# Kernel tuning notes

Measured on AMD Instinct MI355X. Metric: run time of the kernel, lower is better.

Reference implementation:

```python
import jax, jax.numpy as jnp
import numpy as np

EPS = 1e-5

def setup_inputs() -> dict:
    key = jax.random.key(0)
    ks = jax.random.split(key, 12)
    b, C, Hx = 8, 1024, 28          # x: (b, C, Hx, Hx); y: (b, C//2, 2*Hx, 2*Hx)
    C2 = C // 2
    r = C2 // 7                      # fc bottleneck = 73
    f32 = jnp.float32
    inp = {
        'y': jax.random.normal(ks[0], (b, C2, 2*Hx, 2*Hx), f32),
        'x': jax.random.normal(ks[1], (b, C, Hx, Hx), f32),
        'fc1_w': jax.random.normal(ks[2], (r, C2), f32) * 0.02,
        'fc2_w': jax.random.normal(ks[3], (C2, r), f32) * 0.02,
        'conv_w': jax.random.normal(ks[4], (C2, C, 1, 1), f32) * 0.02,
        'conv_b': jnp.zeros((C2,), f32),
        'conv1_w': jax.random.normal(ks[5], (C2, C2 * 4, 1, 1), f32) * 0.02,
        'conv1_b': jnp.zeros((C2,), f32),
        'bn_gamma': jnp.ones((C2,), f32),
        'bn_beta': jnp.zeros((C2,), f32),
        'bn_mean': jnp.zeros((C2,), f32),
        'bn_var': jnp.ones((C2,), f32),
        'dw_w': jax.random.normal(ks[6], (C, 1, 3, 3), f32) * 0.1,  # depthwise, groups=C
        'dw_b': jnp.zeros((C,), f32),
    }
    return inp

def reference(y, x, fc1_w, fc2_w, conv_w, conv_b, conv1_w, conv1_b,
              bn_gamma, bn_beta, bn_mean, bn_var, dw_w, dw_b):
    def bn(t):  # BatchNorm2d in eval mode (running stats); same bn module reused twice
        return (t - bn_mean[:, None, None]) * jax.lax.rsqrt(bn_var[:, None, None] + EPS) \
               * bn_gamma[:, None, None] + bn_beta[:, None, None]
    # SE channel attention on y
    s = jnp.mean(y, axis=(2, 3))                              # (b, C2) GAP
    s = jax.nn.relu(s @ fc1_w.T) @ fc2_w.T                    # bias-free FCs
    y1 = y * jax.nn.sigmoid(s)[:, :, None, None]
    # depthwise 3x3 conv on x
    x1 = jax.lax.conv_general_dilated(
        x, dw_w, (1, 1), ((1, 1), (1, 1)),
        feature_group_count=x.shape[1],
        dimension_numbers=('NCHW', 'OIHW', 'NCHW')) + dw_b[None, :, None, None]
    # np.cov per (b, c) map: rows are variables, ddof=1 -> (Xc @ Xc^T)/(W-1)
    Wn = x1.shape[-1]
    xc = x1 - jnp.mean(x1, axis=-1, keepdims=True)
    x2 = jnp.einsum('bchw,bcgw->bchg', xc, xc) / (Wn - 1)     # (b, C, H, H)
    # 1x1 conv C->C2, bn, sigmoid
    x2 = jnp.einsum('bchw,oc->bohw', x2, conv_w[:, :, 0, 0]) + conv_b[None, :, None, None]
    x2 = jax.nn.sigmoid(bn(x2))
    # bilinear upsample x2 (half-pixel == torch align_corners=False)
    def up2(t):
        bb, cc, hh, ww = t.shape
        return jax.image.resize(t, (bb, cc, 2 * hh, 2 * ww), method='bilinear')
    x_up = up2(x)
    x2_up = up2(x2)
    cat = jnp.concatenate([y1, x2_up, x_up], axis=1)          # (b, 4*C2, 2H, 2W)
    out = jnp.einsum('bchw,oc->bohw', cat, conv1_w[:, :, 0, 0]) + conv1_b[None, :, None, None]
    return jax.nn.relu(bn(out))
```

## Files before the change

kernel.cpp:

```cpp
#include <hip/hip_runtime.h>
#include <math.h>

#define EPSV 1e-5f
#define B 8
#define C 1024
#define C2 512
#define RK 73
#define HW 784
#define QW 3136

typedef __attribute__((ext_vector_type(8))) short bf16x8;
typedef __attribute__((ext_vector_type(4))) float f32x4;

__device__ __forceinline__ unsigned short f2bf(float f) {
    unsigned u = __float_as_uint(f);
    return (unsigned short)((u + 0x7fffu + ((u >> 16) & 1u)) >> 16);
}
__device__ __forceinline__ float ld_f(const float* p) { return *p; }
__device__ __forceinline__ float ld_f(const unsigned short* p) {
    return __uint_as_float(((unsigned)*p) << 16);
}

__global__ void zero_s0(float* __restrict__ s0) {
    s0[blockIdx.x * 256 + threadIdx.x] = 0.f;
}

__global__ void se_fc_kernel(const float* __restrict__ s0,
                             const float* __restrict__ fc1_w,
                             const float* __restrict__ fc2_w,
                             float* __restrict__ att) {
    int b = blockIdx.x;
    __shared__ float sv[C2];
    __shared__ float hv[RK];
    for (int i = threadIdx.x; i < C2; i += 256) sv[i] = s0[b * C2 + i] * (1.0f / QW);
    __syncthreads();
    if (threadIdx.x < RK) {
        float acc = 0.f;
        const float4* wr4 = (const float4*)(fc1_w + threadIdx.x * C2);
        const float4* sv4 = (const float4*)sv;
#pragma unroll 16
        for (int k = 0; k < C2 / 4; ++k) {
            float4 w4 = wr4[k], s4 = sv4[k];
            acc += w4.x * s4.x + w4.y * s4.y + w4.z * s4.z + w4.w * s4.w;
        }
        hv[threadIdx.x] = fmaxf(acc, 0.f);
    }
    __syncthreads();
    for (int o = threadIdx.x; o < C2; o += 256) {
        float acc = 0.f;
        const float* wr = fc2_w + o * RK;
#pragma unroll
        for (int j = 0; j < RK; ++j) acc += wr[j] * hv[j];
        att[b * C2 + o] = 1.f / (1.f + expf(-acc));
    }
}

__global__ void dwcov_kernel(const float* __restrict__ x,
                             const float* __restrict__ dw_w,
                             const float* __restrict__ dw_b,
                             unsigned short* __restrict__ cov) {
    int bc = blockIdx.x;
    int c = bc & (C - 1);
    __shared__ float xs[HW];
    __shared__ float x1[HW];
    __shared__ float rm[28];
    const float* px = x + (size_t)bc * HW;
    for (int i = threadIdx.x; i < HW; i += 256) xs[i] = px[i];
    float wk[9];
#pragma unroll
    for (int j = 0; j < 9; ++j) wk[j] = dw_w[c * 9 + j];
    float bias = dw_b[c];
    __syncthreads();
    for (int p = threadIdx.x; p < HW; p += 256) {
        int h = p / 28, w = p - h * 28;
        float acc = bias;
#pragma unroll
        for (int dh = 0; dh < 3; ++dh) {
            int hh = h + dh - 1;
            if (hh < 0 || hh >= 28) continue;
#pragma unroll
            for (int dw = 0; dw < 3; ++dw) {
                int ww = w + dw - 1;
                if (ww < 0 || ww >= 28) continue;
                acc += xs[hh * 28 + ww] * wk[dh * 3 + dw];
            }
        }
        x1[p] = acc;
    }
    __syncthreads();
    if (threadIdx.x < 28) {
        float s = 0.f;
        for (int w = 0; w < 28; ++w) s += x1[threadIdx.x * 28 + w];
        rm[threadIdx.x] = s * (1.f / 28.f);
    }
    __syncthreads();
    unsigned short* pc = cov + (size_t)bc * HW;
    for (int p = threadIdx.x; p < HW; p += 256) {
        int h = p / 28, g = p - h * 28;
        float mh = rm[h], mg = rm[g];
        float acc = 0.f;
        for (int w = 0; w < 28; ++w)
            acc += (x1[h * 28 + w] - mh) * (x1[g * 28 + w] - mg);
        pc[p] = f2bf(acc * (1.f / 27.f));
    }
}

__global__ void pack_w(const float* __restrict__ conv_w, const float* __restrict__ conv_b,
                       const float* __restrict__ conv1_w, const float* __restrict__ conv1_b,
                       const float* __restrict__ bn_g, const float* __restrict__ bn_b,
                       const float* __restrict__ bn_m, const float* __restrict__ bn_v,
                       const float* __restrict__ att,
                       unsigned short* __restrict__ w0b, unsigned short* __restrict__ w1y,
                       unsigned short* __restrict__ w1pT,
                       float* __restrict__ sA, float* __restrict__ sB0, float* __restrict__ sB1) {
    int o = blockIdx.x, t = threadIdx.x;
    for (int i = t; i < C; i += 256) w0b[(size_t)o * C + i] = f2bf(conv_w[(size_t)o * C + i]);
    for (int i = t; i < 1536; i += 256) w1pT[(size_t)o * 1536 + i] = f2bf(conv1_w[(size_t)o * 2048 + 512 + i]);
#pragma unroll
    for (int b = 0; b < B; ++b)
        for (int c2 = t; c2 < C2; c2 += 256)
            w1y[((size_t)b * C2 + o) * C2 + c2] = f2bf(conv1_w[(size_t)o * 2048 + c2] * att[b * C2 + c2]);
    if (t == 0) {
        float sc = rsqrtf(bn_v[o] + EPSV) * bn_g[o];
        float bi = bn_b[o] - bn_m[o] * sc;
        sA[o] = sc;
        sB0[o] = conv_b[o] * sc + bi;
        sB1[o] = conv1_b[o] * sc + bi;
    }
}

template<typename ST, bool GAP>
__global__ __launch_bounds__(256)
void transpose_pass(const ST* __restrict__ src, unsigned short* __restrict__ dst,
                    float* __restrict__ s0,
                    int rows, int cols, int dpitch, int doff) {
    int b = blockIdx.z;
    int c0 = blockIdx.y * 64, p0 = blockIdx.x * 64;
    __shared__ float ts[64][65];
    int tid = threadIdx.x;
    int pl = tid & 63, r0 = tid >> 6;
    const ST* sb = src + ((size_t)b * rows + c0) * cols + p0;
    if (p0 + pl < cols) {
#pragma unroll
        for (int j = 0; j < 16; ++j) {
            int cl = r0 + j * 4;
            ts[cl][pl] = ld_f(&sb[(size_t)cl * cols + pl]);
        }
    }
    __syncthreads();
    int pl2b = tid >> 3, cl0 = (tid & 7) * 8;
#pragma unroll
    for (int j = 0; j < 2; ++j) {
        int pl2 = pl2b + j * 32;
        if (p0 + pl2 < cols) {
            unsigned short pk[8];
#pragma unroll
            for (int i = 0; i < 8; ++i) pk[i] = f2bf(ts[cl0 + i][pl2]);
            *(uint4*)&dst[((size_t)b * cols + p0 + pl2) * dpitch + doff + c0 + cl0] = *(uint4*)pk;
        }
    }
    if (GAP) {
        if (tid < 64) {
            float s = 0.f;
#pragma unroll
            for (int i = 0; i < 64; ++i) s += ts[tid][i];
            atomicAdd(&s0[b * rows + c0 + tid], s);
        }
    }
}

template<int MODE, int K>
__global__ __launch_bounds__(256)
void mfma_gemm(const unsigned short* __restrict__ wpk,
               const unsigned short* __restrict__ bsrc,
               const unsigned short* __restrict__ Pb,
               const float* __restrict__ sA, const float* __restrict__ sB,
               void* __restrict__ outv) {
    constexpr int NIT = K / 32;
    constexpr int NT  = (MODE == 2) ? 49 : 98;
    constexpr int QN = NT >> 3, REM = NT & 7;
    int bx = blockIdx.x;
    int r = bx & 7, ii = bx >> 3;
    int og = ii & 7, s = ii >> 3;
    int cnt = QN + (r < REM ? 1 : 0);
    if (s >= cnt) return;
    int t = (r < REM ? r * (QN + 1) : REM * (QN + 1) + (r - REM) * QN) + s;
    int o0 = og * 64;
    int n0 = t * 64;
    int b = blockIdx.z;
    union SM {
        struct { __align__(16) unsigned short Wt[2][2048]; __align__(16) unsigned short At[2][2048]; } s;
        float pt[(MODE == 2) ? 64 * 84 : 4];
    };
    __shared__ SM sm;
    int tid = threadIdx.x;
    int lane = tid & 63, wv = tid >> 6;
    int ln = lane & 15, quad = lane >> 4;
    int o_w = (wv >> 1) * 32, q_w = (wv & 1) * 32;
    int swr = tid >> 2, swk = (tid & 3) * 8;
    int stw = swr * 32 + (((tid & 3) ^ ((swr >> 1) & 3)) << 3);
    int rq  = (quad ^ ((ln >> 1) & 3)) << 3;
    const unsigned short* wp = (MODE == 2) ? wpk + (size_t)b * C2 * C2 : wpk;
    const unsigned short* wg = wp + (size_t)(o0 + swr) * K + swk;
    const unsigned short* bg = bsrc + ((size_t)((MODE == 2) ? b * QW : 0) + n0 + swr) * K + swk;

    uint4 stA_a, stA_b, stB_a, stB_b;

#define LD_STAGE(P, CH) {                                                   \
        P##_a = *(const uint4*)(wg + (size_t)(CH) * 32);                    \
        P##_b = *(const uint4*)(bg + (size_t)(CH) * 32); }

#define ST_STAGE(P, BUF) {                                                  \
        *(uint4*)&sm.s.Wt[BUF][stw] = P##_a;                                \
        *(uint4*)&sm.s.At[BUF][stw] = P##_b; }

#define GEMM_BODY(BUF, P, CHW, CHL) {                                               \
        bf16x8 af0 = *(const bf16x8*)&sm.s.Wt[BUF][(o_w + ln) * 32 + rq];           \
        bf16x8 af1 = *(const bf16x8*)&sm.s.Wt[BUF][(o_w + 16 + ln) * 32 + rq];      \
        bf16x8 bf0 = *(const bf16x8*)&sm.s.At[BUF][(q_w + ln) * 32 + rq];           \
        bf16x8 bf1 = *(const bf16x8*)&sm.s.At[BUF][(q_w + 16 + ln) * 32 + rq];      \
        acc[0][0] = __builtin_amdgcn_mfma_f32_16x16x32_bf16(af0, bf0, acc[0][0], 0, 0, 0); \
        acc[0][1] = __builtin_amdgcn_mfma_f32_16x16x32_bf16(af0, bf1, acc[0][1], 0, 0, 0); \
        acc[1][0] = __builtin_amdgcn_mfma_f32_16x16x32_bf16(af1, bf0, acc[1][0], 0, 0, 0); \
        acc[1][1] = __builtin_amdgcn_mfma_f32_16x16x32_bf16(af1, bf1, acc[1][1], 0, 0, 0); \
        if ((CHW) < NIT) {                                                          \
            ST_STAGE(P, (BUF) ^ 1)                                                  \
            if ((CHL) < NIT) LD_STAGE(P, (CHL))                                     \
            asm volatile("s_waitcnt lgkmcnt(0)" ::: "memory");                      \
            __builtin_amdgcn_s_barrier();                                           \
            __builtin_amdgcn_sched_barrier(0);                                      \
        } }

    LD_STAGE(stA, 0)
    ST_STAGE(stA, 0)
    LD_STAGE(stA, 1)
    LD_STAGE(stB, 2)
    asm volatile("s_waitcnt lgkmcnt(0)" ::: "memory");
    __builtin_amdgcn_s_barrier();
    __builtin_amdgcn_sched_barrier(0);

    f32x4 acc[2][2] = {};
    for (int i2 = 0; i2 < NIT; i2 += 2) {
        GEMM_BODY(0, stA, i2 + 1, i2 + 3)
        GEMM_BODY(1, stB, i2 + 2, i2 + 4)
    }
#undef GEMM_BODY
#undef ST_STAGE
#undef LD_STAGE

    if (MODE == 2) {
        float* outp = (float*)outv;
        int h0 = n0 / 56;
        int hmin = (h0 & 1) ? (h0 >> 1) : max(0, (h0 >> 1) - 1);
        float stv[21];
#pragma unroll
        for (int j = 0; j < 21; ++j) {
            int e = tid + j * 256;
            int o_l = e / 84, rem = e - o_l * 84;
            int s2 = rem / 28, w = rem - s2 * 28;
            int row = min(hmin + s2, 27);
            stv[j] = ld_f(&Pb[((size_t)b * C2 + o0 + o_l) * HW + row * 28 + w]);
        }
        __syncthreads();
#pragma unroll
        for (int j = 0; j < 21; ++j) sm.pt[tid + j * 256] = stv[j];
        __syncthreads();
#pragma unroll
        for (int nt = 0; nt < 2; ++nt) {
            int q = n0 + q_w + nt * 16 + ln;
            int hq = q / 56, wq = q - hq * 56;
            int hm = hq >> 1, wm = wq >> 1;
            int hn = (hq & 1) ? min(hm + 1, 27) : max(hm - 1, 0);
            int wn_ = (wq & 1) ? min(wm + 1, 27) : max(wm - 1, 0);
            int rm_ = (hm - hmin) * 28, rn_ = (hn - hmin) * 28;
#pragma unroll
            for (int mt = 0; mt < 2; ++mt)
#pragma unroll
                for (int reg = 0; reg < 4; ++reg) {
                    int ol = o_w + mt * 16 + quad * 4 + reg;
                    int o = o0 + ol;
                    const float* Pt = &sm.pt[ol * 84];
                    float up = 0.5625f * Pt[rm_ + wm] + 0.1875f * (Pt[rm_ + wn_] + Pt[rn_ + wm])
                             + 0.0625f * Pt[rn_ + wn_];
                    float v = (acc[mt][nt][reg] + up) * sA[o] + sB[o];
                    outp[((size_t)b * C2 + o) * QW + q] = fmaxf(v, 0.f);
                }
        }
    } else if (MODE == 0) {
        unsigned short* outp = (unsigned short*)outv;
#pragma unroll
        for (int nt = 0; nt < 2; ++nt) {
            int n = n0 + q_w + nt * 16 + ln;
#pragma unroll
            for (int mt = 0; mt < 2; ++mt) {
                int ob = o0 + o_w + mt * 16 + quad * 4;
                unsigned short pk[4];
#pragma unroll
                for (int reg = 0; reg < 4; ++reg) {
                    int o = ob + reg;
                    float v = acc[mt][nt][reg] * sA[o] + sB[o];
                    pk[reg] = f2bf(1.f / (1.f + expf(-v)));
                }
                *(uint2*)&outp[(size_t)n * 1536 + ob] = *(uint2*)pk;
            }
        }
    } else {
        unsigned short* outp = (unsigned short*)outv;
#pragma unroll
        for (int nt = 0; nt < 2; ++nt) {
            int n = n0 + q_w + nt * 16 + ln;
            int be = n / HW, pe = n - be * HW;
#pragma unroll
            for (int mt = 0; mt < 2; ++mt)
#pragma unroll
                for (int reg = 0; reg < 4; ++reg) {
                    int o = o0 + o_w + mt * 16 + quad * 4 + reg;
                    outp[((size_t)be * C2 + o) * HW + pe] = f2bf(acc[mt][nt][reg]);
                }
        }
    }
}

extern "C" void kernel_launch(void* const* d_in, const int* in_sizes, int n_in,
                              void* d_out, int out_size, void* d_ws, size_t ws_size,
                              hipStream_t stream) {
    const float* y       = (const float*)d_in[0];
    const float* x       = (const float*)d_in[1];
    const float* fc1_w   = (const float*)d_in[2];
    const float* fc2_w   = (const float*)d_in[3];
    const float* conv_w  = (const float*)d_in[4];
    const float* conv_b  = (const float*)d_in[5];
    const float* conv1_w = (const float*)d_in[6];
    const float* conv1_b = (const float*)d_in[7];
    const float* bn_g    = (const float*)d_in[8];
    const float* bn_b    = (const float*)d_in[9];
    const float* bn_m    = (const float*)d_in[10];
    const float* bn_v    = (const float*)d_in[11];
    const float* dw_w    = (const float*)d_in[12];
    const float* dw_b    = (const float*)d_in[13];
    float* out = (float*)d_out;

    unsigned short* cov_bf = (unsigned short*)d_out;
    unsigned short* covT   = cov_bf + (size_t)B * C * HW;
    unsigned short* BcatT  = covT + (size_t)B * HW * C;

    float* ws  = (float*)d_ws;
    float* s0  = ws;
    float* att = ws + 4096;
    float* sA  = ws + 8192;
    float* sB0 = ws + 8704;
    float* sB1 = ws + 9216;
    unsigned short* w0b  = (unsigned short*)(ws + 9728);
    unsigned short* w1y  = w0b + (size_t)C2 * C;
    unsigned short* w1pT = w1y + (size_t)B * C2 * C2;
    unsigned short* yT   = w1pT + (size_t)C2 * 1536;
    unsigned short* Pb   = yT + (size_t)B * QW * C2;

    zero_s0<<<16, 256, 0, stream>>>(s0);
    transpose_pass<float, true><<<dim3(49, 8, B), 256, 0, stream>>>(
        y, yT, s0, C2, QW, C2, 0);
    se_fc_kernel<<<B, 256, 0, stream>>>(s0, fc1_w, fc2_w, att);
    pack_w<<<C2, 256, 0, stream>>>(conv_w, conv_b, conv1_w, conv1_b,
                                   bn_g, bn_b, bn_m, bn_v, att,
                                   w0b, w1y, w1pT, sA, sB0, sB1);
    dwcov_kernel<<<B * C, 256, 0, stream>>>(x, dw_w, dw_b, cov_bf);
    transpose_pass<float, false><<<dim3(13, 16, B), 256, 0, stream>>>(
        x, BcatT, nullptr, C, HW, 1536, 512);
    transpose_pass<unsigned short, false><<<dim3(13, 16, B), 256, 0, stream>>>(
        cov_bf, covT, nullptr, C, HW, C, 0);
    mfma_gemm<0, 1024><<<dim3(832), 256, 0, stream>>>(w0b, covT, nullptr, sA, sB0, BcatT);
    mfma_gemm<1, 1536><<<dim3(832), 256, 0, stream>>>(w1pT, BcatT, nullptr, sA, sB0, Pb);
    mfma_gemm<2, 512><<<dim3(448, 1, B), 256, 0, stream>>>(w1y, yT, Pb, sA, sB1, out);
}
```

Before: 307.4 us.

## Vectorize loads in cov, weight packing, transpose, deepen GEMM register prefetch

Several independent changes land together. The covariance loop reads LDS rows as float4, and pack_w converts weights with float4 loads and packed stores. The transpose loads four elements per thread, and the GEMM's register prefetch deepens from two to four in-flight stages. The aim is fewer memory instructions and more latency hiding on global loads, at the cost of more VGPRs in the GEMM and the assumption that NIT is a multiple of 4.

```diff
diff --git a/kernel.cpp b/kernel.cpp
--- a/kernel.cpp
+++ b/kernel.cpp
@@ -19,6 +19,17 @@
 __device__ __forceinline__ float ld_f(const float* p) { return *p; }
 __device__ __forceinline__ float ld_f(const unsigned short* p) {
     return __uint_as_float(((unsigned)*p) << 16);
+}
+__device__ __forceinline__ void ld4f(const float* p, float* d) {
+    float4 v = *(const float4*)p;
+    d[0] = v.x; d[1] = v.y; d[2] = v.z; d[3] = v.w;
+}
+__device__ __forceinline__ void ld4f(const unsigned short* p, float* d) {
+    uint2 u = *(const uint2*)p;
+    d[0] = __uint_as_float((u.x & 0xffffu) << 16);
+    d[1] = __uint_as_float(u.x & 0xffff0000u);
+    d[2] = __uint_as_float((u.y & 0xffffu) << 16);
+    d[3] = __uint_as_float(u.y & 0xffff0000u);
 }
 
 __global__ void zero_s0(float* __restrict__ s0) {
@@ -62,7 +73,7 @@
     int bc = blockIdx.x;
     int c = bc & (C - 1);
     __shared__ float xs[HW];
-    __shared__ float x1[HW];
+    __shared__ __align__(16) float x1[HW];
     __shared__ float rm[28];
     const float* px = x + (size_t)bc * HW;
     for (int i = threadIdx.x; i < HW; i += 256) xs[i] = px[i];
@@ -98,9 +109,17 @@
     for (int p = threadIdx.x; p < HW; p += 256) {
         int h = p / 28, g = p - h * 28;
         float mh = rm[h], mg = rm[g];
+        const float4* xh = (const float4*)&x1[h * 28];
+        const float4* xg = (const float4*)&x1[g * 28];
         float acc = 0.f;
-        for (int w = 0; w < 28; ++w)
-            acc += (x1[h * 28 + w] - mh) * (x1[g * 28 + w] - mg);
+#pragma unroll
+        for (int w4 = 0; w4 < 7; ++w4) {
+            float4 a = xh[w4], bq = xg[w4];
+            acc += (a.x - mh) * (bq.x - mg);
+            acc += (a.y - mh) * (bq.y - mg);
+            acc += (a.z - mh) * (bq.z - mg);
+            acc += (a.w - mh) * (bq.w - mg);
+        }
         pc[p] = f2bf(acc * (1.f / 27.f));
     }
 }
@@ -114,12 +133,32 @@
                        unsigned short* __restrict__ w1pT,
                        float* __restrict__ sA, float* __restrict__ sB0, float* __restrict__ sB1) {
     int o = blockIdx.x, t = threadIdx.x;
-    for (int i = t; i < C; i += 256) w0b[(size_t)o * C + i] = f2bf(conv_w[(size_t)o * C + i]);
-    for (int i = t; i < 1536; i += 256) w1pT[(size_t)o * 1536 + i] = f2bf(conv1_w[(size_t)o * 2048 + 512 + i]);
-#pragma unroll
-    for (int b = 0; b < B; ++b)
-        for (int c2 = t; c2 < C2; c2 += 256)
-            w1y[((size_t)b * C2 + o) * C2 + c2] = f2bf(conv1_w[(size_t)o * 2048 + c2] * att[b * C2 + c2]);
+    {
+        int c4 = t * 4;
+        float4 w4 = *(const float4*)&conv_w[(size_t)o * C + c4];
+        unsigned short pk[4] = { f2bf(w4.x), f2bf(w4.y), f2bf(w4.z), f2bf(w4.w) };
+        *(uint2*)&w0b[(size_t)o * C + c4] = *(uint2*)pk;
+    }
+#pragma unroll
+    for (int i = 0; i < 2; ++i) {
+        int e = t + i * 256;
+        if (e < 384) {
+            int c4 = e * 4;
+            float4 w4 = *(const float4*)&conv1_w[(size_t)o * 2048 + 512 + c4];
+            unsigned short pk[4] = { f2bf(w4.x), f2bf(w4.y), f2bf(w4.z), f2bf(w4.w) };
+            *(uint2*)&w1pT[(size_t)o * 1536 + c4] = *(uint2*)pk;
+        }
+    }
+#pragma unroll
+    for (int i = 0; i < 4; ++i) {
+        int e = t + i * 256;
+        int bb = e >> 7, c4 = (e & 127) * 4;
+        float4 w4 = *(const float4*)&conv1_w[(size_t)o * 2048 + c4];
+        float4 a4 = *(const float4*)&att[bb * C2 + c4];
+        unsigned short pk[4] = { f2bf(w4.x * a4.x), f2bf(w4.y * a4.y),
+                                 f2bf(w4.z * a4.z), f2bf(w4.w * a4.w) };
+        *(uint2*)&w1y[((size_t)bb * C2 + o) * C2 + c4] = *(uint2*)pk;
+    }
     if (t == 0) {
         float sc = rsqrtf(bn_v[o] + EPSV) * bn_g[o];
         float bi = bn_b[o] - bn_m[o] * sc;
@@ -138,13 +177,16 @@
     int c0 = blockIdx.y * 64, p0 = blockIdx.x * 64;
     __shared__ float ts[64][65];
     int tid = threadIdx.x;
-    int pl = tid & 63, r0 = tid >> 6;
+    int pl4 = (tid & 15) * 4, rr = tid >> 4;
     const ST* sb = src + ((size_t)b * rows + c0) * cols + p0;
-    if (p0 + pl < cols) {
-#pragma unroll
-        for (int j = 0; j < 16; ++j) {
-            int cl = r0 + j * 4;
-            ts[cl][pl] = ld_f(&sb[(size_t)cl * cols + pl]);
+    if (p0 + pl4 < cols) {
+#pragma unroll
+        for (int j = 0; j < 4; ++j) {
+            int cl = rr + j * 16;
+            float d[4];
+            ld4f(&sb[(size_t)cl * cols + pl4], d);
+            ts[cl][pl4 + 0] = d[0]; ts[cl][pl4 + 1] = d[1];
+            ts[cl][pl4 + 2] = d[2]; ts[cl][pl4 + 3] = d[3];
         }
     }
     __syncthreads();
@@ -204,7 +246,7 @@
     const unsigned short* wg = wp + (size_t)(o0 + swr) * K + swk;
     const unsigned short* bg = bsrc + ((size_t)((MODE == 2) ? b * QW : 0) + n0 + swr) * K + swk;
 
-    uint4 stA_a, stA_b, stB_a, stB_b;
+    uint4 stA_a, stA_b, stB_a, stB_b, stC_a, stC_b, stD_a, stD_b;
 
 #define LD_STAGE(P, CH) {                                                   \
         P##_a = *(const uint4*)(wg + (size_t)(CH) * 32);                    \
@@ -233,16 +275,20 @@
 
     LD_STAGE(stA, 0)
     ST_STAGE(stA, 0)
-    LD_STAGE(stA, 1)
-    LD_STAGE(stB, 2)
+    LD_STAGE(stB, 1)
+    LD_STAGE(stC, 2)
+    LD_STAGE(stD, 3)
+    LD_STAGE(stA, 4)
     asm volatile("s_waitcnt lgkmcnt(0)" ::: "memory");
     __builtin_amdgcn_s_barrier();
     __builtin_amdgcn_sched_barrier(0);
 
     f32x4 acc[2][2] = {};
-    for (int i2 = 0; i2 < NIT; i2 += 2) {
-        GEMM_BODY(0, stA, i2 + 1, i2 + 3)
-        GEMM_BODY(1, stB, i2 + 2, i2 + 4)
+    for (int i2 = 0; i2 < NIT; i2 += 4) {
+        GEMM_BODY(0, stB, i2 + 1, i2 + 5)
+        GEMM_BODY(1, stC, i2 + 2, i2 + 6)
+        GEMM_BODY(0, stD, i2 + 3, i2 + 7)
+        GEMM_BODY(1, stA, i2 + 4, i2 + 8)
     }
 #undef GEMM_BODY
 #undef ST_STAGE
```

Result: faster. 294.4 us (-4.2%).
